# Optimization experiments

Hardware: AMD Instinct MI355X
Metric: run time of the kernel (lower is better)

The kernel has to match this reference:

```python
import jax, jax.numpy as jnp
import numpy as np

C_QKV = 128
C_HID = 32
N_HEADS = 4
INF = 1e9


def setup_inputs() -> dict:
    key = jax.random.key(0)
    ks = jax.random.split(key, 8)
    B, S = 256, 256
    hc = N_HEADS * C_HID  # 128
    inp = {
        "input_qkv": jax.random.normal(ks[0], (1, B, S, C_QKV), dtype=jnp.float32),
        "mask": jnp.ones((1, B, 1, 1, S), dtype=jnp.float32),
        "bias": jax.random.normal(ks[1], (1, 1, N_HEADS, S, S), dtype=jnp.float32),
        "add_transposed_output_to": jax.random.normal(ks[2], (1, B, S, C_QKV), dtype=jnp.float32),
        # linear_qkvg: Linear(c_qkv, 4*h*c), bias=False -> weight [4*hc, c_qkv]
        "W_qkvg": jax.random.normal(ks[3], (4 * hc, C_QKV), dtype=jnp.float32) * (1.0 / np.sqrt(C_QKV)),
        # gating bias initialized to ones in the module
        "linear_g_bias": jnp.ones((hc,), dtype=jnp.float32),
        # linear_o: Linear(hc, c_qkv), init='final' (zeros in AF2, use small random for a nontrivial test)
        "W_o": jax.random.normal(ks[4], (C_QKV, hc), dtype=jnp.float32) * (1.0 / np.sqrt(hc)),
        "b_o": jax.random.normal(ks[5], (C_QKV,), dtype=jnp.float32) * 0.02,
    }
    return inp


def reference(input_qkv, mask, bias, add_transposed_output_to, W_qkvg, linear_g_bias, W_o, b_o):
    hc = N_HEADS * C_HID
    # fused QKVG projection: [1, b, s, 4*hc]
    qkvg = jnp.einsum("xbsc,fc->xbsf", input_qkv, W_qkvg)
    q, k, v, g = jnp.split(qkvg, 4, axis=-1)
    # reshape to heads: [1, b, s, h, c]
    shp = q.shape[:-1] + (N_HEADS, C_HID)
    q = q.reshape(shp)
    k = k.reshape(shp)
    v = v.reshape(shp)
    scale = 1.0 / np.sqrt(C_HID)
    # scores: [1, b, h, q, k]
    a = jnp.einsum("xbqhc,xbkhc->xbhqk", q * scale, k)
    a = a + (mask - 1.0) * INF + bias
    a = jax.nn.softmax(a, axis=-1)
    # attention output: [1, b, q, h, c] -> [1, b, s, hc]
    o = jnp.einsum("xbhqk,xbkhc->xbqhc", a, v)
    o = o.reshape(o.shape[:-2] + (hc,))
    # sigmoid gating
    o = o * jax.nn.sigmoid(g + linear_g_bias)
    # fused linear + transpose(-2,-3) + add
    proj = jnp.einsum("xbsf,of->xbso", o, W_o) + b_o  # [1, b, s, c_qkv]
    out = add_transposed_output_to + jnp.swapaxes(proj, -2, -3)  # [1, s, b, c_qkv]
    return out
```

## Files before the change

### kernel.cpp

```cpp
#include <hip/hip_runtime.h>
#include <math.h>

#define BB 256
#define SS 256
#define NH 4

typedef __attribute__((ext_vector_type(8))) short bfrag;
typedef __attribute__((ext_vector_type(4))) float ffrag;

__device__ inline unsigned short f2bf(float x) {
    unsigned u = __float_as_uint(x);
    u += 0x7FFF + ((u >> 16) & 1);
    return (unsigned short)(u >> 16);
}
__device__ inline float bf2f(unsigned short h) {
    return __uint_as_float(((unsigned)h) << 16);
}
__device__ inline unsigned pack2(float a, float b) {
    return (unsigned)f2bf(a) | ((unsigned)f2bf(b) << 16);
}
union FragU { unsigned u[4]; bfrag b; };

#define XB_OFF  0
#define WB_OFF  8388608
#define WOB_OFF 8454144
#define OG_OFF  8470528

__global__ __launch_bounds__(256) void k0_cast(
    const float* __restrict__ X, const float* __restrict__ W,
    const float* __restrict__ Wo, unsigned short* __restrict__ dst)
{
    const int gid = blockIdx.x * 256 + threadIdx.x;
    const int XN8 = 8388608 / 8, WN8 = 65536 / 8, WoN8 = 16384 / 8;
    const float* src;
    size_t soff, doff;
    if (gid < XN8)            { src = X;  soff = (size_t)gid * 8;                 doff = XB_OFF + soff; }
    else if (gid < XN8 + WN8) { src = W;  soff = (size_t)(gid - XN8) * 8;         doff = WB_OFF + soff; }
    else if (gid < XN8 + WN8 + WoN8) { src = Wo; soff = (size_t)(gid - XN8 - WN8) * 8; doff = WOB_OFF + soff; }
    else return;
    const float4 a = *(const float4*)(src + soff);
    const float4 b = *(const float4*)(src + soff + 4);
    unsigned r0 = pack2(a.x, a.y), r1 = pack2(a.z, a.w);
    unsigned r2 = pack2(b.x, b.y), r3 = pack2(b.z, b.w);
    uint4 o; o.x = r0; o.y = r1; o.z = r2; o.w = r3;
    *(uint4*)(dst + doff) = o;
}

__global__ __launch_bounds__(256, 2) void k_fused(
    const unsigned short* __restrict__ Xb,
    const unsigned short* __restrict__ Wb,
    const float* __restrict__ gbias,
    const float* __restrict__ mask,
    const float* __restrict__ bias,
    unsigned short* __restrict__ og)
{
    const int h = blockIdx.x, b = blockIdx.y;
    const int t = threadIdx.x;
    const int w = t >> 6, lane = t & 63, l15 = lane & 15, quad = lane >> 4;

    __shared__ unsigned short Qb[SS * 40];
    __shared__ unsigned short Kb[SS * 40];
    __shared__ unsigned short Vt[32 * 264];
    __shared__ unsigned short Gb[SS * 34];
    __shared__ float maskLds[SS];

    maskLds[t] = (mask[b * SS + t] - 1.0f) * 1e9f;

    const float qscale = 0.17677669529663687f;

    for (int half = 0; half < 2; ++half) {
        bfrag Wfr[4][4];
#pragma unroll
        for (int f4 = 0; f4 < 4; ++f4) {
            const int floc = (half * 4 + f4) * 16 + l15;
            const int grow = (floc >> 5) * 128 + h * 32 + (floc & 31);
#pragma unroll
            for (int cc = 0; cc < 4; ++cc)
                Wfr[f4][cc] = *(const bfrag*)(Wb + grow * 128 + cc * 32 + quad * 8);
        }
#pragma unroll
        for (int st = 0; st < 4; ++st) {
            const int s = w * 64 + st * 16 + l15;
            bfrag Xfr[4];
#pragma unroll
            for (int cc = 0; cc < 4; ++cc)
                Xfr[cc] = *(const bfrag*)(Xb + (b * SS + s) * 128 + cc * 32 + quad * 8);
#pragma unroll
            for (int f4 = 0; f4 < 4; ++f4) {
                ffrag D = {0.f, 0.f, 0.f, 0.f};
#pragma unroll
                for (int cc = 0; cc < 4; ++cc)
                    D = __builtin_amdgcn_mfma_f32_16x16x32_bf16(Xfr[cc], Wfr[f4][cc], D, 0, 0, 0);
                const int ft = half * 4 + f4;
                const int fcol = ft * 16 + l15;
                const int srow0 = w * 64 + st * 16 + quad * 4;
                if (ft < 2) {
#pragma unroll
                    for (int r = 0; r < 4; ++r)
                        Qb[(srow0 + r) * 40 + fcol] = f2bf(D[r] * qscale);
                } else if (ft < 4) {
#pragma unroll
                    for (int r = 0; r < 4; ++r)
                        Kb[(srow0 + r) * 40 + (fcol - 32)] = f2bf(D[r]);
                } else if (ft < 6) {
                    const int base = (fcol - 64) * 264 + srow0;
                    *(unsigned*)&Vt[base]     = pack2(D[0], D[1]);
                    *(unsigned*)&Vt[base + 2] = pack2(D[2], D[3]);
                } else {
                    const int c = fcol - 96;
                    const float gb = gbias[h * 32 + c];
#pragma unroll
                    for (int r = 0; r < 4; ++r) {
                        const float g = 1.0f / (1.0f + __expf(-(D[r] + gb)));
                        Gb[(srow0 + r) * 34 + c] = f2bf(g);
                    }
                }
            }
        }
    }
    __syncthreads();

    bfrag Vfr[2][8];
#pragma unroll
    for (int ch = 0; ch < 2; ++ch)
#pragma unroll
        for (int ck = 0; ck < 8; ++ck)
            Vfr[ch][ck] = *(const bfrag*)&Vt[(ch * 16 + l15) * 264 + ck * 32 + quad * 8];

    const int srcA = l15 + ((quad & 1) * 2) * 16;
    const int srcB = srcA + 16;
    const bool hi = (quad >> 1) != 0;

    for (int qq = 0; qq < 4; ++qq) {
        const int q = w * 64 + qq * 16 + l15;
        const bfrag Qfr = *(const bfrag*)&Qb[q * 40 + quad * 8];

        ffrag S[16];
#pragma unroll
        for (int kt = 0; kt < 16; ++kt) {
            const bfrag Kfr = *(const bfrag*)&Kb[(kt * 16 + l15) * 40 + quad * 8];
            const ffrag z = {0.f, 0.f, 0.f, 0.f};
            S[kt] = __builtin_amdgcn_mfma_f32_16x16x32_bf16(Kfr, Qfr, z, 0, 0, 0);
        }

        const float* brow = bias + (h * SS + q) * SS;
        float m = -1e30f;
#pragma unroll
        for (int kt = 0; kt < 16; ++kt) {
            const float4 bv = *(const float4*)(brow + kt * 16 + quad * 4);
            const float4 mv = *(const float4*)(maskLds + kt * 16 + quad * 4);
            S[kt][0] += bv.x + mv.x; S[kt][1] += bv.y + mv.y;
            S[kt][2] += bv.z + mv.z; S[kt][3] += bv.w + mv.w;
            m = fmaxf(m, fmaxf(fmaxf(S[kt][0], S[kt][1]), fmaxf(S[kt][2], S[kt][3])));
        }
        m = fmaxf(m, __shfl_xor(m, 16, 64));
        m = fmaxf(m, __shfl_xor(m, 32, 64));

        float l = 0.f;
        unsigned pk[16][2];
#pragma unroll
        for (int kt = 0; kt < 16; ++kt) {
            const float p0 = __expf(S[kt][0] - m);
            const float p1 = __expf(S[kt][1] - m);
            const float p2 = __expf(S[kt][2] - m);
            const float p3 = __expf(S[kt][3] - m);
            l += (p0 + p1) + (p2 + p3);
            pk[kt][0] = pack2(p0, p1);
            pk[kt][1] = pack2(p2, p3);
        }
        l += __shfl_xor(l, 16, 64);
        l += __shfl_xor(l, 32, 64);

        ffrag O[2];
        O[0] = (ffrag){0.f, 0.f, 0.f, 0.f};
        O[1] = (ffrag){0.f, 0.f, 0.f, 0.f};
#pragma unroll
        for (int ck = 0; ck < 8; ++ck) {
            const unsigned a0 = (unsigned)__shfl((int)pk[2 * ck][0],     srcA, 64);
            const unsigned b0 = (unsigned)__shfl((int)pk[2 * ck + 1][0], srcA, 64);
            const unsigned a1 = (unsigned)__shfl((int)pk[2 * ck][1],     srcA, 64);
            const unsigned b1 = (unsigned)__shfl((int)pk[2 * ck + 1][1], srcA, 64);
            const unsigned a2 = (unsigned)__shfl((int)pk[2 * ck][0],     srcB, 64);
            const unsigned b2 = (unsigned)__shfl((int)pk[2 * ck + 1][0], srcB, 64);
            const unsigned a3 = (unsigned)__shfl((int)pk[2 * ck][1],     srcB, 64);
            const unsigned b3 = (unsigned)__shfl((int)pk[2 * ck + 1][1], srcB, 64);
            FragU fu;
            fu.u[0] = hi ? b0 : a0;
            fu.u[1] = hi ? b1 : a1;
            fu.u[2] = hi ? b2 : a2;
            fu.u[3] = hi ? b3 : a3;
            O[0] = __builtin_amdgcn_mfma_f32_16x16x32_bf16(Vfr[0][ck], fu.b, O[0], 0, 0, 0);
            O[1] = __builtin_amdgcn_mfma_f32_16x16x32_bf16(Vfr[1][ck], fu.b, O[1], 0, 0, 0);
        }

        const float invl = 1.0f / l;
        const unsigned short* gr = &Gb[q * 34];
        unsigned* orow = (unsigned*)(og + (b * SS + q) * 128 + h * 32);
#pragma unroll
        for (int ch = 0; ch < 2; ++ch) {
            const int c0 = ch * 16 + quad * 4;
            const float v0 = O[ch][0] * invl * bf2f(gr[c0 + 0]);
            const float v1 = O[ch][1] * invl * bf2f(gr[c0 + 1]);
            const float v2 = O[ch][2] * invl * bf2f(gr[c0 + 2]);
            const float v3 = O[ch][3] * invl * bf2f(gr[c0 + 3]);
            orow[(c0 >> 1) + 0] = pack2(v0, v1);
            orow[(c0 >> 1) + 1] = pack2(v2, v3);
        }
    }
}

__global__ __launch_bounds__(256, 4) void k3_proj(
    const unsigned short* __restrict__ ogb,
    const unsigned short* __restrict__ Wob,
    const float* __restrict__ bo,
    const float* __restrict__ addt,
    float* __restrict__ out)
{
    const int j = blockIdx.x, ih = blockIdx.y;
    const int t = threadIdx.x;
    const int w = t >> 6, lane = t & 63, l15 = lane & 15, quad = lane >> 4;

    __shared__ unsigned short OgS[128 * 136];

    {
        const int ss = t >> 1, hf = t & 1;
        const unsigned short* src = ogb + (((size_t)j * SS + ih * 128 + ss) * 128) + hf * 64;
        unsigned short* dst = &OgS[ss * 136 + hf * 64];
#pragma unroll
        for (int u = 0; u < 8; ++u)
            *(uint4*)(dst + u * 8) = *(const uint4*)(src + u * 8);
    }

    bfrag Wfr[2][4];
#pragma unroll
    for (int ctl = 0; ctl < 2; ++ctl) {
        const int crow = (w * 2 + ctl) * 16 + l15;
#pragma unroll
        for (int cc = 0; cc < 4; ++cc)
            Wfr[ctl][cc] = *(const bfrag*)(Wob + crow * 128 + cc * 32 + quad * 8);
    }
    const float bo0 = bo[(w * 2 + 0) * 16 + l15];
    const float bo1 = bo[(w * 2 + 1) * 16 + l15];

    __syncthreads();

#pragma unroll
    for (int jt = 0; jt < 8; ++jt) {
        bfrag Ab[4];
#pragma unroll
        for (int cc = 0; cc < 4; ++cc)
            Ab[cc] = *(const bfrag*)&OgS[(jt * 16 + l15) * 136 + cc * 32 + quad * 8];

        ffrag D0 = {0.f, 0.f, 0.f, 0.f};
        ffrag D1 = {0.f, 0.f, 0.f, 0.f};
#pragma unroll
        for (int cc = 0; cc < 4; ++cc) {
            D0 = __builtin_amdgcn_mfma_f32_16x16x32_bf16(Ab[cc], Wfr[0][cc], D0, 0, 0, 0);
            D1 = __builtin_amdgcn_mfma_f32_16x16x32_bf16(Ab[cc], Wfr[1][cc], D1, 0, 0, 0);
        }

        const int c0 = (w * 2 + 0) * 16 + l15;
        const int c1 = (w * 2 + 1) * 16 + l15;
#pragma unroll
        for (int r = 0; r < 4; ++r) {
            const int s = ih * 128 + jt * 16 + quad * 4 + r;
            const size_t row = ((size_t)s * BB + j) * 128;
            out[row + c0] = D0[r] + bo0 + addt[row + c0];
            out[row + c1] = D1[r] + bo1 + addt[row + c1];
        }
    }
}

extern "C" void kernel_launch(void* const* d_in, const int* in_sizes, int n_in,
                              void* d_out, int out_size, void* d_ws, size_t ws_size,
                              hipStream_t stream) {
    const float* X     = (const float*)d_in[0];
    const float* mask  = (const float*)d_in[1];
    const float* bias  = (const float*)d_in[2];
    const float* addt  = (const float*)d_in[3];
    const float* Wqkvg = (const float*)d_in[4];
    const float* gbias = (const float*)d_in[5];
    const float* Wo    = (const float*)d_in[6];
    const float* bo    = (const float*)d_in[7];
    float* out = (float*)d_out;

    unsigned short* ws = (unsigned short*)d_ws;
    unsigned short* Xb  = ws + XB_OFF;
    unsigned short* Wb  = ws + WB_OFF;
    unsigned short* Wob = ws + WOB_OFF;
    unsigned short* og  = ws + OG_OFF;

    k0_cast<<<4136, 256, 0, stream>>>(X, Wqkvg, Wo, ws);
    k_fused<<<dim3(NH, BB), 256, 0, stream>>>(Xb, Wb, gbias, mask, bias, og);
    k3_proj<<<dim3(BB, 2), 256, 0, stream>>>(og, Wob, bo, addt, out);
}
```

Before: 232.9 us.

## Fuse output projection into attention kernel via last-block atomic counter

Removes the separate projection kernel. Each attention block bumps a per-batch global counter, and the fourth (last) head block for a batch runs the W_o projection, bias add and transposed residual add for all 256 rows of that batch. The counter is reset in the cast kernel. This saves a kernel launch and lets the projection overlap with other attention blocks. In exchange, the projection work is serialized onto one block per batch, that block re-reads og from global/L2 instead of LDS, and threadfence/atomic overhead is added.

```diff
diff --git a/kernel.cpp b/kernel.cpp
--- a/kernel.cpp
+++ b/kernel.cpp
@@ -21,6 +21,8 @@
 }
 union FragU { unsigned u[4]; bfrag b; };
 
+__device__ int g_cnt[BB];
+
 #define XB_OFF  0
 #define WB_OFF  8388608
 #define WOB_OFF 8454144
@@ -30,6 +32,7 @@
     const float* __restrict__ X, const float* __restrict__ W,
     const float* __restrict__ Wo, unsigned short* __restrict__ dst)
 {
+    if (blockIdx.x == 0 && threadIdx.x < BB) g_cnt[threadIdx.x] = 0;
     const int gid = blockIdx.x * 256 + threadIdx.x;
     const int XN8 = 8388608 / 8, WN8 = 65536 / 8, WoN8 = 16384 / 8;
     const float* src;
@@ -52,7 +55,11 @@
     const float* __restrict__ gbias,
     const float* __restrict__ mask,
     const float* __restrict__ bias,
-    unsigned short* __restrict__ og)
+    unsigned short* __restrict__ og,
+    const unsigned short* __restrict__ Wob,
+    const float* __restrict__ bo,
+    const float* __restrict__ addt,
+    float* __restrict__ out)
 {
     const int h = blockIdx.x, b = blockIdx.y;
     const int t = threadIdx.x;
@@ -63,6 +70,7 @@
     __shared__ unsigned short Vt[32 * 264];
     __shared__ unsigned short Gb[SS * 34];
     __shared__ float maskLds[SS];
+    __shared__ int lastFlag;
 
     maskLds[t] = (mask[b * SS + t] - 1.0f) * 1e9f;
 
@@ -207,66 +215,51 @@
             orow[(c0 >> 1) + 1] = pack2(v2, v3);
         }
     }
-}
-
-__global__ __launch_bounds__(256, 4) void k3_proj(
-    const unsigned short* __restrict__ ogb,
-    const unsigned short* __restrict__ Wob,
-    const float* __restrict__ bo,
-    const float* __restrict__ addt,
-    float* __restrict__ out)
-{
-    const int j = blockIdx.x, ih = blockIdx.y;
-    const int t = threadIdx.x;
-    const int w = t >> 6, lane = t & 63, l15 = lane & 15, quad = lane >> 4;
-
-    __shared__ unsigned short OgS[128 * 136];
-
-    {
-        const int ss = t >> 1, hf = t & 1;
-        const unsigned short* src = ogb + (((size_t)j * SS + ih * 128 + ss) * 128) + hf * 64;
-        unsigned short* dst = &OgS[ss * 136 + hf * 64];
-#pragma unroll
-        for (int u = 0; u < 8; ++u)
-            *(uint4*)(dst + u * 8) = *(const uint4*)(src + u * 8);
-    }
-
-    bfrag Wfr[2][4];
-#pragma unroll
-    for (int ctl = 0; ctl < 2; ++ctl) {
-        const int crow = (w * 2 + ctl) * 16 + l15;
-#pragma unroll
-        for (int cc = 0; cc < 4; ++cc)
-            Wfr[ctl][cc] = *(const bfrag*)(Wob + crow * 128 + cc * 32 + quad * 8);
-    }
-    const float bo0 = bo[(w * 2 + 0) * 16 + l15];
-    const float bo1 = bo[(w * 2 + 1) * 16 + l15];
-
+
+    __threadfence();
     __syncthreads();
-
-#pragma unroll
-    for (int jt = 0; jt < 8; ++jt) {
-        bfrag Ab[4];
-#pragma unroll
-        for (int cc = 0; cc < 4; ++cc)
-            Ab[cc] = *(const bfrag*)&OgS[(jt * 16 + l15) * 136 + cc * 32 + quad * 8];
-
-        ffrag D0 = {0.f, 0.f, 0.f, 0.f};
-        ffrag D1 = {0.f, 0.f, 0.f, 0.f};
-#pragma unroll
-        for (int cc = 0; cc < 4; ++cc) {
-            D0 = __builtin_amdgcn_mfma_f32_16x16x32_bf16(Ab[cc], Wfr[0][cc], D0, 0, 0, 0);
-            D1 = __builtin_amdgcn_mfma_f32_16x16x32_bf16(Ab[cc], Wfr[1][cc], D1, 0, 0, 0);
-        }
-
-        const int c0 = (w * 2 + 0) * 16 + l15;
-        const int c1 = (w * 2 + 1) * 16 + l15;
-#pragma unroll
-        for (int r = 0; r < 4; ++r) {
-            const int s = ih * 128 + jt * 16 + quad * 4 + r;
-            const size_t row = ((size_t)s * BB + j) * 128;
-            out[row + c0] = D0[r] + bo0 + addt[row + c0];
-            out[row + c1] = D1[r] + bo1 + addt[row + c1];
+    if (t == 0) {
+        const int old = atomicAdd(&g_cnt[b], 1);
+        lastFlag = (old == 3) ? 1 : 0;
+    }
+    __syncthreads();
+    if (lastFlag) {
+        __threadfence();
+
+        bfrag Wfr2[2][4];
+#pragma unroll
+        for (int ctl = 0; ctl < 2; ++ctl) {
+            const int crow = (w * 2 + ctl) * 16 + l15;
+#pragma unroll
+            for (int cc = 0; cc < 4; ++cc)
+                Wfr2[ctl][cc] = *(const bfrag*)(Wob + crow * 128 + cc * 32 + quad * 8);
+        }
+        const float bo0 = bo[(w * 2 + 0) * 16 + l15];
+        const float bo1 = bo[(w * 2 + 1) * 16 + l15];
+
+        for (int jt = 0; jt < 16; ++jt) {
+            bfrag Ab[4];
+#pragma unroll
+            for (int cc = 0; cc < 4; ++cc)
+                Ab[cc] = *(const bfrag*)(og + ((size_t)(b * SS + jt * 16 + l15)) * 128 + cc * 32 + quad * 8);
+
+            ffrag D0 = {0.f, 0.f, 0.f, 0.f};
+            ffrag D1 = {0.f, 0.f, 0.f, 0.f};
+#pragma unroll
+            for (int cc = 0; cc < 4; ++cc) {
+                D0 = __builtin_amdgcn_mfma_f32_16x16x32_bf16(Ab[cc], Wfr2[0][cc], D0, 0, 0, 0);
+                D1 = __builtin_amdgcn_mfma_f32_16x16x32_bf16(Ab[cc], Wfr2[1][cc], D1, 0, 0, 0);
+            }
+
+            const int c0 = (w * 2 + 0) * 16 + l15;
+            const int c1 = (w * 2 + 1) * 16 + l15;
+#pragma unroll
+            for (int r = 0; r < 4; ++r) {
+                const int s = jt * 16 + quad * 4 + r;
+                const size_t row = ((size_t)s * BB + b) * 128;
+                out[row + c0] = (D0[r] + bo0) + addt[row + c0];
+                out[row + c1] = (D1[r] + bo1) + addt[row + c1];
+            }
         }
     }
 }
@@ -291,6 +284,6 @@
     unsigned short* og  = ws + OG_OFF;
 
     k0_cast<<<4136, 256, 0, stream>>>(X, Wqkvg, Wo, ws);
-    k_fused<<<dim3(NH, BB), 256, 0, stream>>>(Xb, Wb, gbias, mask, bias, og);
-    k3_proj<<<dim3(BB, 2), 256, 0, stream>>>(og, Wob, bo, addt, out);
-}
+    k_fused<<<dim3(NH, BB), 256, 0, stream>>>(Xb, Wb, gbias, mask, bias, og,
+                                              Wob, bo, addt, out);
+}
```

New measurement: 532.6 us. 129% more time.
